# Optimization experiments

Hardware: AMD Instinct MI355X
Metric: run time of the kernel (lower is better)

## Reference

```python
import jax, jax.numpy as jnp
import numpy as np

B, T, D, V = 32, 512, 512, 512


def setup_inputs() -> dict:
    key = jax.random.key(0)
    k1, k2, k3, k4 = jax.random.split(key, 4)
    x = jax.random.normal(k1, (B, T, D), jnp.float32)
    proj_w = jax.random.normal(k2, (V, D), jnp.float32) * 0.02
    transitions = jax.random.normal(k3, (V, V), jnp.float32) * 0.02
    tgt_tokens = jax.random.randint(k4, (B, T), 0, V, dtype=jnp.int64)
    decoder_padding_mask = jnp.zeros((B, T), dtype=bool)  # all positions valid
    return {"x": x, "proj_w": proj_w, "transitions": transitions,
            "tgt_tokens": tgt_tokens, "decoder_padding_mask": decoder_padding_mask}


def reference(x, proj_w, transitions, tgt_tokens, decoder_padding_mask):
    # output projection (no bias): emissions [B,T,V]
    emissions = jnp.einsum('btd,vd->btv', x, proj_w)
    mask = (~decoder_padding_mask).astype(emissions.dtype)  # [B,T] word_ins_mask

    alpha0 = emissions[:, 0]                                # [B,V]
    emit_rest = jnp.swapaxes(emissions[:, 1:], 0, 1)        # [T-1,B,V]
    mask_rest = jnp.swapaxes(mask[:, 1:], 0, 1)             # [T-1,B]

    # ---- CRF forward algorithm (log partition) ----
    def fwd_step(alpha, inp):
        emit_t, m_t = inp
        # scores[b,i,j] = alpha[b,i] + trans[i,j] + emit_t[b,j]
        scores = alpha[:, :, None] + transitions[None, :, :] + emit_t[:, None, :]
        new = jax.nn.logsumexp(scores, axis=1)
        return jnp.where(m_t[:, None] > 0, new, alpha), None

    alpha_T, _ = jax.lax.scan(fwd_step, alpha0, (emit_rest, mask_rest))
    logZ = jax.nn.logsumexp(alpha_T, axis=-1)               # [B]

    # ---- gold path score ----
    emit_scores = jnp.take_along_axis(emissions, tgt_tokens[..., None], axis=-1)[..., 0]
    score = jnp.sum(emit_scores * mask, axis=-1)
    trans_scores = transitions[tgt_tokens[:, :-1], tgt_tokens[:, 1:]]  # [B,T-1]
    score = score + jnp.sum(trans_scores * mask[:, 1:] * mask[:, :-1], axis=-1)
    loglik = score - logZ                                   # [B]

    # ---- Viterbi decode ----
    lab = jnp.arange(V)

    def vit_step(alpha, inp):
        emit_t, m_t = inp
        scores = alpha[:, :, None] + transitions[None, :, :]  # [B,V,V]
        best_prev = jnp.argmax(scores, axis=1)                # [B,V]
        new = jnp.max(scores, axis=1) + emit_t
        alpha_new = jnp.where(m_t[:, None] > 0, new, alpha)
        bp = jnp.where(m_t[:, None] > 0, best_prev, lab[None, :])
        return alpha_new, bp

    valpha, bps = jax.lax.scan(vit_step, alpha0, (emit_rest, mask_rest))  # bps [T-1,B,V]
    last = jnp.argmax(valpha, axis=-1)                      # [B] token at T-1

    def back_step(tok_next, bp_t):
        tok_prev = jnp.take_along_axis(bp_t, tok_next[:, None], axis=1)[:, 0]
        return tok_prev, tok_next

    first, later = jax.lax.scan(back_step, last, bps, reverse=True)
    tokens = jnp.concatenate([first[:, None], jnp.swapaxes(later, 0, 1)], axis=1)  # [B,T]

    return emissions, loglik, tokens
```

## Files before the change

kernel.cpp:

```cpp
#include <hip/hip_runtime.h>

#define Bn 32
#define Tn 512
#define Dn 512
#define Vn 512

typedef float f4 __attribute__((ext_vector_type(4)));
typedef int i8v __attribute__((ext_vector_type(8)));
typedef _Float16 h8f __attribute__((ext_vector_type(8)));

__device__ __forceinline__ float max8lds(const float* p) {
  float4 a = *(const float4*)p;
  float4 b = *(const float4*)(p + 4);
  return fmaxf(fmaxf(fmaxf(a.x, a.y), fmaxf(a.z, a.w)),
               fmaxf(fmaxf(b.x, b.y), fmaxf(b.z, b.w)));
}

__device__ __forceinline__ float dpp64max(float x) {
  int t;
  t = __builtin_amdgcn_update_dpp(__float_as_int(x), __float_as_int(x), 0x111, 0xF, 0xF, false);
  x = fmaxf(x, __int_as_float(t));
  t = __builtin_amdgcn_update_dpp(__float_as_int(x), __float_as_int(x), 0x112, 0xF, 0xF, false);
  x = fmaxf(x, __int_as_float(t));
  t = __builtin_amdgcn_update_dpp(__float_as_int(x), __float_as_int(x), 0x114, 0xF, 0xF, false);
  x = fmaxf(x, __int_as_float(t));
  t = __builtin_amdgcn_update_dpp(__float_as_int(x), __float_as_int(x), 0x118, 0xF, 0xF, false);
  x = fmaxf(x, __int_as_float(t));
  t = __builtin_amdgcn_update_dpp(__float_as_int(x), __float_as_int(x), 0x142, 0xF, 0xF, false);
  x = fmaxf(x, __int_as_float(t));
  t = __builtin_amdgcn_update_dpp(__float_as_int(x), __float_as_int(x), 0x143, 0xF, 0xF, false);
  x = fmaxf(x, __int_as_float(t));
  return __int_as_float(__builtin_amdgcn_readlane(__float_as_int(x), 63));
}

__device__ __forceinline__ void bar_lgkm() {
  asm volatile("s_waitcnt lgkmcnt(0)" ::: "memory");
  __builtin_amdgcn_s_barrier();
}

__device__ __forceinline__ unsigned int f32_to_e4m3(float x) {
  x = fminf(x, 448.0f);
  unsigned int bits = __float_as_uint(x);
  int e = (int)((bits >> 23) & 0xFF) - 127;
  if (e < -6) {
    return (unsigned int)__float2int_rn(x * 512.0f);
  }
  unsigned int man = bits & 0x7FFFFF;
  int te = e + 7;
  unsigned int r = man >> 20;
  unsigned int rem = man & 0xFFFFF;
  if (rem > 0x80000u || (rem == 0x80000u && (r & 1u))) r++;
  if (r == 8u) { r = 0u; te++; }
  if (te > 15) { te = 15; r = 6u; }
  unsigned int byte = ((unsigned int)te << 3) | r;
  if (byte > 0x7Eu) byte = 0x7Eu;
  return byte;
}

__global__ __launch_bounds__(512) void crf_minmax(const float* __restrict__ trans,
                                                  unsigned int* __restrict__ Rout) {
  __shared__ float smn[8][64], smx[8][64];
  const int c = threadIdx.x & 63;
  const int seg = threadIdx.x >> 6;
  const int col = (int)blockIdx.x * 64 + c;
  float mn = 3e38f, mx = -3e38f;
#pragma unroll 4
  for (int u = seg * 64; u < seg * 64 + 64; ++u) {
    float t = trans[(size_t)u * Vn + col];
    mn = fminf(mn, t); mx = fmaxf(mx, t);
  }
  smn[seg][c] = mn; smx[seg][c] = mx;
  __syncthreads();
  if (seg == 0) {
#pragma unroll
    for (int i = 1; i < 8; ++i) { mn = fminf(mn, smn[i][c]); mx = fmaxf(mx, smx[i][c]); }
    float r = dpp64max(mx - mn);
    if (c == 0) atomicMax((int*)Rout, __float_as_int(r));
  }
}

__global__ __launch_bounds__(256) void crf_build_E8(const float* __restrict__ trans,
                                                    unsigned char* __restrict__ E8) {
  const int fid = (int)blockIdx.x;
  const int vt = fid >> 2, kc = fid & 3;
  const int t = threadIdx.x;
  const int lane = t >> 2;
  const int j0 = (t & 3) * 8;
  const int v = vt * 16 + (lane & 15);
  const int ubase = kc * 128 + (lane >> 4) * 32 + j0;
  unsigned long long pack = 0;
#pragma unroll
  for (int s = 0; s < 8; ++s) {
    float e = __expf(trans[(size_t)(ubase + s) * Vn + v]);
    pack |= (unsigned long long)f32_to_e4m3(e) << (8 * s);
  }
  *(unsigned long long*)(E8 + (size_t)fid * 2048 + lane * 32 + j0) = pack;
}

__global__ __launch_bounds__(256) void crf_gemm(const float* __restrict__ X,
                                                const float* __restrict__ Wt,
                                                float* __restrict__ C) {
  __shared__ h8f XfH[4][64], XfL[4][64];
  __shared__ h8f WfH[32][64], WfL[32][64];
  const int tid = threadIdx.x;
  const int m0 = (int)blockIdx.x * 64;
  const int wv = tid >> 6, lane = tid & 63;
  const int g = lane >> 4, cc = lane & 15;
  const int srow = tid >> 2;
  const int sc0 = (tid & 3) * 8;
  const int p = (tid & 3) * 16 + ((tid >> 2) & 15);
  f4 acc[32];
#pragma unroll
  for (int i = 0; i < 32; ++i) acc[i] = (f4)(0.f);

  for (int k0 = 0; k0 < Dn; k0 += 32) {
    __syncthreads();
    {
      const float* xp = X + (size_t)(m0 + srow) * Dn + k0 + sc0;
      float4 xa = *(const float4*)xp;
      float4 xb = *(const float4*)(xp + 4);
      float xs[8] = {xa.x, xa.y, xa.z, xa.w, xb.x, xb.y, xb.z, xb.w};
      _Float16 hh[8], ll[8];
#pragma unroll
      for (int i = 0; i < 8; ++i) {
        hh[i] = (_Float16)xs[i];
        ll[i] = (_Float16)(xs[i] - (float)hh[i]);
      }
      XfH[tid >> 6][p] = *(h8f*)hh;
      XfL[tid >> 6][p] = *(h8f*)ll;
#pragma unroll
      for (int i = 0; i < 8; ++i) {
        int r = i * 64 + srow;
        const float* wp = Wt + (size_t)r * Dn + k0 + sc0;
        float4 wa = *(const float4*)wp;
        float4 wb = *(const float4*)(wp + 4);
        float wsv[8] = {wa.x, wa.y, wa.z, wa.w, wb.x, wb.y, wb.z, wb.w};
        _Float16 wh[8], wl[8];
#pragma unroll
        for (int q = 0; q < 8; ++q) {
          wh[q] = (_Float16)wsv[q];
          wl[q] = (_Float16)(wsv[q] - (float)wh[q]);
        }
        WfH[i * 4 + (tid >> 6)][p] = *(h8f*)wh;
        WfL[i * 4 + (tid >> 6)][p] = *(h8f*)wl;
      }
    }
    __syncthreads();
    h8f aH = XfH[wv][lane];
    h8f aL = XfL[wv][lane];
#pragma unroll
    for (int nt = 0; nt < 32; ++nt) {
      h8f bH = WfH[nt][lane];
      h8f bL = WfL[nt][lane];
      acc[nt] = __builtin_amdgcn_mfma_f32_16x16x32_f16(aH, bH, acc[nt], 0, 0, 0);
      acc[nt] = __builtin_amdgcn_mfma_f32_16x16x32_f16(aH, bL, acc[nt], 0, 0, 0);
      acc[nt] = __builtin_amdgcn_mfma_f32_16x16x32_f16(aL, bH, acc[nt], 0, 0, 0);
      acc[nt] = __builtin_amdgcn_mfma_f32_16x16x32_f16(aL, bL, acc[nt], 0, 0, 0);
    }
  }
#pragma unroll
  for (int nt = 0; nt < 32; ++nt)
#pragma unroll
    for (int r = 0; r < 4; ++r)
      C[(size_t)(m0 + wv * 16 + 4 * g + r) * Vn + nt * 16 + cc] = acc[nt][r];
}

union SM {
  struct {
    __align__(16) unsigned char ph[Vn];
    __align__(16) float wred[8];
    __align__(16) float wred2[8];
    unsigned char padsh[Tn];
  } f;
  struct {
    __align__(16) float va2[2][Vn];
    __align__(16) unsigned short bpbuf[32][Vn];
    unsigned short tokens[Tn];
    __align__(16) float wvals[8];
    int widxs[8];
    unsigned char padsh[Tn];
    int lastS;
  } v;
};

__global__ __launch_bounds__(512, 2) void crf_scan(
    const float* __restrict__ emis, const float* __restrict__ trans,
    const unsigned char* __restrict__ E8, const float* __restrict__ Rp,
    const int* __restrict__ tgt, const unsigned char* __restrict__ pad,
    unsigned short* __restrict__ bps, float* __restrict__ out_ll,
    float* __restrict__ out_tok) {
  __shared__ SM sm;

  const int tid = threadIdx.x;
  const int b = blockIdx.x & 31;
  const int role = blockIdx.x >> 5;
  const float* eb = emis + (size_t)b * Tn * Vn;
  const int w = tid >> 6;
  const int lane = tid & 63;

  if (role == 0) {
    const int g = lane >> 4, c = lane & 15;
    const int t2sel = c >> 2, r2sel = c & 3;
    const int sidx = ((16 * ((lane >> 2) & 3)) + 4 * (lane >> 4) + (lane & 3)) << 2;
    i8v EA[4][4];
    {
      const i8v* E8v = (const i8v*)E8;
#pragma unroll
      for (int vt2 = 0; vt2 < 4; ++vt2)
#pragma unroll
        for (int kc = 0; kc < 4; ++kc)
          EA[vt2][kc] = E8v[((4 * w + vt2) * 4 + kc) * 64 + lane];
    }
    sm.f.padsh[tid] = pad[b * Tn + tid];
    float alphaR = eb[tid];
    float ecur = eb[Vn + tid];
    {
      float r = dpp64max(alphaR);
      if (lane == 0) sm.f.wred[w] = r;
    }
    bar_lgkm();
    float m = max8lds(sm.f.wred);

    for (int t = 1; t < Tn; ++t) {
      float p = __expf(alphaR - m);
      sm.f.ph[tid] = (unsigned char)f32_to_e4m3(p);
      bar_lgkm();
      float enext = (t + 1 < Tn) ? eb[(size_t)(t + 1) * Vn + tid] : 0.f;
      const uint4* phq = (const uint4*)sm.f.ph;
      i8v B4[4];
#pragma unroll
      for (int kc = 0; kc < 4; ++kc) {
        union { uint4 u[2]; i8v v; } bu;
        bu.u[0] = phq[kc * 8 + g * 2];
        bu.u[1] = phq[kc * 8 + g * 2 + 1];
        B4[kc] = bu.v;
      }
      f4 acc0 = (f4)(0.f), acc1 = (f4)(0.f), acc2 = (f4)(0.f), acc3 = (f4)(0.f);
#pragma unroll
      for (int kc = 0; kc < 4; ++kc) {
        acc0 = __builtin_amdgcn_mfma_scale_f32_16x16x128_f8f6f4(
            EA[0][kc], B4[kc], acc0, 0, 0, 0, 0x7F7F7F7F, 0, 0x7F7F7F7F);
        acc1 = __builtin_amdgcn_mfma_scale_f32_16x16x128_f8f6f4(
            EA[1][kc], B4[kc], acc1, 0, 0, 0, 0x7F7F7F7F, 0, 0x7F7F7F7F);
        acc2 = __builtin_amdgcn_mfma_scale_f32_16x16x128_f8f6f4(
            EA[2][kc], B4[kc], acc2, 0, 0, 0, 0x7F7F7F7F, 0, 0x7F7F7F7F);
        acc3 = __builtin_amdgcn_mfma_scale_f32_16x16x128_f8f6f4(
            EA[3][kc], B4[kc], acc3, 0, 0, 0, 0x7F7F7F7F, 0, 0x7F7F7F7F);
      }
      f4 at = (t2sel == 0) ? acc0 : (t2sel == 1) ? acc1 : (t2sel == 2) ? acc2 : acc3;
      float lo = (r2sel & 1) ? at[1] : at[0];
      float hi = (r2sel & 1) ? at[3] : at[2];
      float tot = (r2sel & 2) ? hi : lo;
      float tv = __int_as_float(__builtin_amdgcn_ds_bpermute(sidx, __float_as_int(tot)));
      float nv = m + __logf(tv) + ecur;
      if (sm.f.padsh[t]) nv = alphaR;
      alphaR = nv; ecur = enext;
      float rmx = dpp64max(nv);
      if (lane == 0) sm.f.wred[w] = rmx;
      bar_lgkm();
      m = max8lds(sm.f.wred);
    }

    __syncthreads();
    float ex = __expf(alphaR - m);
#pragma unroll
    for (int off = 1; off < 64; off <<= 1) ex += __shfl_xor(ex, off);
    if (lane == 0) sm.f.wred[w] = ex;
    float sc;
    {
      int t = tid;
      int tg = tgt[b * Tn + t];
      float mt = sm.f.padsh[t] ? 0.f : 1.f;
      sc = eb[(size_t)t * Vn + tg] * mt;
      if (t < Tn - 1) {
        int tg1 = tgt[b * Tn + t + 1];
        float mt1 = sm.f.padsh[t + 1] ? 0.f : 1.f;
        sc += trans[(size_t)tg * Vn + tg1] * mt * mt1;
      }
    }
#pragma unroll
    for (int off = 1; off < 64; off <<= 1) sc += __shfl_xor(sc, off);
    if (lane == 0) sm.f.wred2[w] = sc;
    __syncthreads();
    if (tid == 0) {
      float s = 0.f, gg = 0.f;
      for (int i = 0; i < 8; ++i) { s += sm.f.wred[i]; gg += sm.f.wred2[i]; }
      out_ll[b] = gg - (m + __logf(s));
    }
  } else {
    float R = __int_as_float(((const int*)Rp)[0]) * 1.000001f + 1e-4f;
    sm.v.padsh[tid] = pad[b * Tn + tid];
    float vaR = eb[tid];
    sm.v.va2[0][tid] = vaR;
    float ecur = eb[Vn + tid];
    bar_lgkm();

    for (int t = 1; t < Tn; ++t) {
      const int cur = t & 1, prev = cur ^ 1;
      const float* va2p = sm.v.va2[prev];
      const float4* vap4 = (const float4*)va2p;
      float4 q0 = vap4[lane * 2];
      float4 q1 = vap4[lane * 2 + 1];
      float mx8 = fmaxf(fmaxf(fmaxf(q0.x, q0.y), fmaxf(q0.z, q0.w)),
                        fmaxf(fmaxf(q1.x, q1.y), fmaxf(q1.z, q1.w)));
      float gmax = dpp64max(mx8);
      float thr = gmax - R;
      unsigned long long bm[8];
      bm[0] = __ballot(q0.x >= thr);
      bm[1] = __ballot(q0.y >= thr);
      bm[2] = __ballot(q0.z >= thr);
      bm[3] = __ballot(q0.w >= thr);
      bm[4] = __ballot(q1.x >= thr);
      bm[5] = __ballot(q1.y >= thr);
      bm[6] = __ballot(q1.z >= thr);
      bm[7] = __ballot(q1.w >= thr);
      unsigned long long any = bm[0] | bm[1] | bm[2] | bm[3] |
                               bm[4] | bm[5] | bm[6] | bm[7];
      float enext = (t + 1 < Tn) ? eb[(size_t)(t + 1) * Vn + tid] : 0.f;
      float best = -3e38f; int arg = 0;
      while (any) {
        int l = __ffsll(any) - 1; any &= any - 1;
#pragma unroll
        for (int j = 0; j < 8; ++j) {
          if ((bm[j] >> l) & 1) {
            int u = 8 * l + j;
            float cnd = va2p[u] + trans[(size_t)u * Vn + tid];
            if (cnd > best) { best = cnd; arg = u; }
          }
        }
      }
      float nv = best + ecur; int bp = arg;
      if (sm.v.padsh[t]) { nv = vaR; bp = tid; }
      bps[((size_t)(t - 1) * Bn + b) * Vn + tid] = (unsigned short)bp;
      sm.v.va2[cur][tid] = nv;
      vaR = nv; ecur = enext;
      bar_lgkm();
    }

    asm volatile("s_waitcnt vmcnt(0)" ::: "memory");
    __syncthreads();

    {
      float val = vaR;
      int idx = tid;
#pragma unroll
      for (int off = 1; off < 64; off <<= 1) {
        float ov = __shfl_xor(val, off);
        int oi = __shfl_xor(idx, off);
        if (ov > val || (ov == val && oi < idx)) { val = ov; idx = oi; }
      }
      if (lane == 0) { sm.v.wvals[w] = val; sm.v.widxs[w] = idx; }
    }
    __syncthreads();
    if (tid == 0) {
      float bv = sm.v.wvals[0]; int bi = sm.v.widxs[0];
      for (int i = 1; i < 8; ++i)
        if (sm.v.wvals[i] > bv || (sm.v.wvals[i] == bv && sm.v.widxs[i] < bi)) {
          bv = sm.v.wvals[i]; bi = sm.v.widxs[i];
        }
      sm.v.lastS = bi;
    }
    __syncthreads();
    int tok = sm.v.lastS;

    for (int cch = 15; cch >= 0; --cch) {
      int rhi = cch * 32 + 31; if (rhi > 510) rhi = 510;
      int srow = tid >> 4, part = tid & 15;
      int row = cch * 32 + srow;
      if (row <= 510) {
        const uint4* src = (const uint4*)(bps + ((size_t)row * Bn + b) * Vn);
        uint4* dst = (uint4*)&sm.v.bpbuf[srow][0];
#pragma unroll
        for (int qq = 0; qq < 4; ++qq) dst[part * 4 + qq] = src[part * 4 + qq];
      }
      __syncthreads();
      if (tid == 0) {
        int tk = tok;
        for (int rr = rhi; rr >= cch * 32; --rr) {
          sm.v.tokens[rr + 1] = (unsigned short)tk;
          tk = sm.v.bpbuf[rr - cch * 32][tk];
        }
        tok = tk;
      }
      __syncthreads();
    }
    if (tid == 0) sm.v.tokens[0] = (unsigned short)tok;
    __syncthreads();
    out_tok[b * Tn + tid] = (float)sm.v.tokens[tid];
  }
}

extern "C" void kernel_launch(void* const* d_in, const int* in_sizes, int n_in,
                              void* d_out, int out_size, void* d_ws, size_t ws_size,
                              hipStream_t stream) {
  const float* x = (const float*)d_in[0];
  const float* w = (const float*)d_in[1];
  const float* trans = (const float*)d_in[2];
  const int* tgt = (const int*)d_in[3];
  const unsigned char* pad = (const unsigned char*)d_in[4];
  float* out = (float*)d_out;

  char* ws = (char*)d_ws;
  float* Rp = (float*)ws;
  unsigned char* E8 = (unsigned char*)(ws + 64);
  unsigned short* bps = (unsigned short*)(ws + 64 + 524288);

  float* emis = out;
  float* out_ll = out + 8388608;
  float* out_tok = out + 8388640;

  (void)hipMemsetAsync(Rp, 0, 4, stream);
  hipLaunchKernelGGL(crf_minmax, dim3(8), dim3(512), 0, stream, trans, (unsigned int*)Rp);
  hipLaunchKernelGGL(crf_build_E8, dim3(128), dim3(256), 0, stream, trans, E8);
  hipLaunchKernelGGL(crf_gemm, dim3(256), dim3(256), 0, stream, x, w, emis);
  hipLaunchKernelGGL(crf_scan, dim3(64), dim3(512), 0, stream, emis, trans, E8, Rp,
                     tgt, pad, bps, out_ll, out_tok);
}
```

Measured before the change: 682.1 us.

## Run Viterbi scan in a single wavefront and use hardware fp8 convert

The Viterbi role now runs on one 64-lane wavefront. Each lane owns 8 states in registers, and LDS holds the alpha vector in a padded layout. This removes the per-step block barriers and lets each lane issue vectorized float4 transition loads and packed 16-byte backpointer stores. Backtracking is also done within the single wave without __syncthreads. Separately, the forward scan swaps the software e4m3 conversion for the hardware cvt_pk_fp8 builtin when it is available. The trade-off is that each Viterbi lane now does 8x the candidate work, and the other 7 waves of that block exit early.

```diff
diff --git a/kernel.cpp b/kernel.cpp
--- a/kernel.cpp
+++ b/kernel.cpp
@@ -55,6 +55,14 @@
   unsigned int byte = ((unsigned int)te << 3) | r;
   if (byte > 0x7Eu) byte = 0x7Eu;
   return byte;
+}
+
+__device__ __forceinline__ unsigned int cvt_e4m3_fast(float p) {
+#if __has_builtin(__builtin_amdgcn_cvt_pk_fp8_f32)
+  return (unsigned int)(__builtin_amdgcn_cvt_pk_fp8_f32(p, p, 0, false) & 0xFF);
+#else
+  return f32_to_e4m3(p);
+#endif
 }
 
 __global__ __launch_bounds__(512) void crf_minmax(const float* __restrict__ trans,
@@ -173,14 +181,11 @@
     unsigned char padsh[Tn];
   } f;
   struct {
-    __align__(16) float va2[2][Vn];
-    __align__(16) unsigned short bpbuf[32][Vn];
+    __align__(16) float va_lds[64 * 9];
+    __align__(16) unsigned short bpbuf[16][Vn];
     unsigned short tokens[Tn];
-    __align__(16) float wvals[8];
-    int widxs[8];
-    unsigned char padsh[Tn];
-    int lastS;
-  } v;
+    unsigned char padv[Tn];
+  } v1;
 };
 
 __global__ __launch_bounds__(512, 2) void crf_scan(
@@ -196,12 +201,12 @@
   const int role = blockIdx.x >> 5;
   const float* eb = emis + (size_t)b * Tn * Vn;
   const int w = tid >> 6;
-  const int lane = tid & 63;
+  const int lane64 = tid & 63;
 
   if (role == 0) {
-    const int g = lane >> 4, c = lane & 15;
+    const int g = lane64 >> 4, c = lane64 & 15;
     const int t2sel = c >> 2, r2sel = c & 3;
-    const int sidx = ((16 * ((lane >> 2) & 3)) + 4 * (lane >> 4) + (lane & 3)) << 2;
+    const int sidx = ((16 * ((lane64 >> 2) & 3)) + 4 * (lane64 >> 4) + (lane64 & 3)) << 2;
     i8v EA[4][4];
     {
       const i8v* E8v = (const i8v*)E8;
@@ -209,21 +214,21 @@
       for (int vt2 = 0; vt2 < 4; ++vt2)
 #pragma unroll
         for (int kc = 0; kc < 4; ++kc)
-          EA[vt2][kc] = E8v[((4 * w + vt2) * 4 + kc) * 64 + lane];
+          EA[vt2][kc] = E8v[((4 * w + vt2) * 4 + kc) * 64 + lane64];
     }
     sm.f.padsh[tid] = pad[b * Tn + tid];
     float alphaR = eb[tid];
     float ecur = eb[Vn + tid];
     {
       float r = dpp64max(alphaR);
-      if (lane == 0) sm.f.wred[w] = r;
+      if (lane64 == 0) sm.f.wred[w] = r;
     }
     bar_lgkm();
     float m = max8lds(sm.f.wred);
 
     for (int t = 1; t < Tn; ++t) {
       float p = __expf(alphaR - m);
-      sm.f.ph[tid] = (unsigned char)f32_to_e4m3(p);
+      sm.f.ph[tid] = (unsigned char)cvt_e4m3_fast(p);
       bar_lgkm();
       float enext = (t + 1 < Tn) ? eb[(size_t)(t + 1) * Vn + tid] : 0.f;
       const uint4* phq = (const uint4*)sm.f.ph;
@@ -256,7 +261,7 @@
       if (sm.f.padsh[t]) nv = alphaR;
       alphaR = nv; ecur = enext;
       float rmx = dpp64max(nv);
-      if (lane == 0) sm.f.wred[w] = rmx;
+      if (lane64 == 0) sm.f.wred[w] = rmx;
       bar_lgkm();
       m = max8lds(sm.f.wred);
     }
@@ -265,7 +270,7 @@
     float ex = __expf(alphaR - m);
 #pragma unroll
     for (int off = 1; off < 64; off <<= 1) ex += __shfl_xor(ex, off);
-    if (lane == 0) sm.f.wred[w] = ex;
+    if (lane64 == 0) sm.f.wred[w] = ex;
     float sc;
     {
       int t = tid;
@@ -280,7 +285,7 @@
     }
 #pragma unroll
     for (int off = 1; off < 64; off <<= 1) sc += __shfl_xor(sc, off);
-    if (lane == 0) sm.f.wred2[w] = sc;
+    if (lane64 == 0) sm.f.wred2[w] = sc;
     __syncthreads();
     if (tid == 0) {
       float s = 0.f, gg = 0.f;
@@ -288,105 +293,122 @@
       out_ll[b] = gg - (m + __logf(s));
     }
   } else {
+    if (tid >= 64) return;
+    const int lane = tid;
     float R = __int_as_float(((const int*)Rp)[0]) * 1.000001f + 1e-4f;
-    sm.v.padsh[tid] = pad[b * Tn + tid];
-    float vaR = eb[tid];
-    sm.v.va2[0][tid] = vaR;
-    float ecur = eb[Vn + tid];
-    bar_lgkm();
+#pragma unroll
+    for (int i = 0; i < 8; ++i)
+      sm.v1.padv[lane * 8 + i] = pad[b * Tn + lane * 8 + i];
+
+    float va[8], ecur[8], enext[8];
+    {
+      float4 a0 = *(const float4*)(eb + lane * 8);
+      float4 a1 = *(const float4*)(eb + lane * 8 + 4);
+      va[0] = a0.x; va[1] = a0.y; va[2] = a0.z; va[3] = a0.w;
+      va[4] = a1.x; va[5] = a1.y; va[6] = a1.z; va[7] = a1.w;
+      float4 e0 = *(const float4*)(eb + Vn + lane * 8);
+      float4 e1 = *(const float4*)(eb + Vn + lane * 8 + 4);
+      ecur[0] = e0.x; ecur[1] = e0.y; ecur[2] = e0.z; ecur[3] = e0.w;
+      ecur[4] = e1.x; ecur[5] = e1.y; ecur[6] = e1.z; ecur[7] = e1.w;
+#pragma unroll
+      for (int j = 0; j < 8; ++j) enext[j] = 0.f;
+    }
+#pragma unroll
+    for (int j = 0; j < 8; ++j) sm.v1.va_lds[9 * lane + j] = va[j];
 
     for (int t = 1; t < Tn; ++t) {
-      const int cur = t & 1, prev = cur ^ 1;
-      const float* va2p = sm.v.va2[prev];
-      const float4* vap4 = (const float4*)va2p;
-      float4 q0 = vap4[lane * 2];
-      float4 q1 = vap4[lane * 2 + 1];
-      float mx8 = fmaxf(fmaxf(fmaxf(q0.x, q0.y), fmaxf(q0.z, q0.w)),
-                        fmaxf(fmaxf(q1.x, q1.y), fmaxf(q1.z, q1.w)));
-      float gmax = dpp64max(mx8);
+      float mx = fmaxf(fmaxf(fmaxf(va[0], va[1]), fmaxf(va[2], va[3])),
+                       fmaxf(fmaxf(va[4], va[5]), fmaxf(va[6], va[7])));
+      float gmax = dpp64max(mx);
       float thr = gmax - R;
       unsigned long long bm[8];
-      bm[0] = __ballot(q0.x >= thr);
-      bm[1] = __ballot(q0.y >= thr);
-      bm[2] = __ballot(q0.z >= thr);
-      bm[3] = __ballot(q0.w >= thr);
-      bm[4] = __ballot(q1.x >= thr);
-      bm[5] = __ballot(q1.y >= thr);
-      bm[6] = __ballot(q1.z >= thr);
-      bm[7] = __ballot(q1.w >= thr);
+#pragma unroll
+      for (int j = 0; j < 8; ++j) bm[j] = __ballot(va[j] >= thr);
       unsigned long long any = bm[0] | bm[1] | bm[2] | bm[3] |
                                bm[4] | bm[5] | bm[6] | bm[7];
-      float enext = (t + 1 < Tn) ? eb[(size_t)(t + 1) * Vn + tid] : 0.f;
-      float best = -3e38f; int arg = 0;
+      if (t + 1 < Tn) {
+        float4 e0 = *(const float4*)(eb + (size_t)(t + 1) * Vn + lane * 8);
+        float4 e1 = *(const float4*)(eb + (size_t)(t + 1) * Vn + lane * 8 + 4);
+        enext[0] = e0.x; enext[1] = e0.y; enext[2] = e0.z; enext[3] = e0.w;
+        enext[4] = e1.x; enext[5] = e1.y; enext[6] = e1.z; enext[7] = e1.w;
+      }
+      float best[8]; int arg[8];
+#pragma unroll
+      for (int j = 0; j < 8; ++j) { best[j] = -3e38f; arg[j] = 0; }
       while (any) {
         int l = __ffsll(any) - 1; any &= any - 1;
 #pragma unroll
         for (int j = 0; j < 8; ++j) {
           if ((bm[j] >> l) & 1) {
             int u = 8 * l + j;
-            float cnd = va2p[u] + trans[(size_t)u * Vn + tid];
-            if (cnd > best) { best = cnd; arg = u; }
+            float vau = sm.v1.va_lds[9 * l + j];
+            const float* tr = trans + (size_t)u * Vn + lane * 8;
+            float4 t0 = *(const float4*)tr;
+            float4 t1 = *(const float4*)(tr + 4);
+            float cc0 = vau + t0.x, cc1 = vau + t0.y, cc2 = vau + t0.z, cc3 = vau + t0.w;
+            float cc4 = vau + t1.x, cc5 = vau + t1.y, cc6 = vau + t1.z, cc7 = vau + t1.w;
+            if (cc0 > best[0]) { best[0] = cc0; arg[0] = u; }
+            if (cc1 > best[1]) { best[1] = cc1; arg[1] = u; }
+            if (cc2 > best[2]) { best[2] = cc2; arg[2] = u; }
+            if (cc3 > best[3]) { best[3] = cc3; arg[3] = u; }
+            if (cc4 > best[4]) { best[4] = cc4; arg[4] = u; }
+            if (cc5 > best[5]) { best[5] = cc5; arg[5] = u; }
+            if (cc6 > best[6]) { best[6] = cc6; arg[6] = u; }
+            if (cc7 > best[7]) { best[7] = cc7; arg[7] = u; }
           }
         }
       }
-      float nv = best + ecur; int bp = arg;
-      if (sm.v.padsh[t]) { nv = vaR; bp = tid; }
-      bps[((size_t)(t - 1) * Bn + b) * Vn + tid] = (unsigned short)bp;
-      sm.v.va2[cur][tid] = nv;
-      vaR = nv; ecur = enext;
-      bar_lgkm();
+      bool pd = sm.v1.padv[t] != 0;
+      __align__(16) unsigned short bp8[8];
+#pragma unroll
+      for (int j = 0; j < 8; ++j) {
+        float nv = best[j] + ecur[j];
+        int bp = arg[j];
+        if (pd) { nv = va[j]; bp = 8 * lane + j; }
+        va[j] = nv;
+        bp8[j] = (unsigned short)bp;
+        ecur[j] = enext[j];
+      }
+      *(uint4*)(bps + ((size_t)(t - 1) * Bn + b) * Vn + lane * 8) = *(const uint4*)bp8;
+#pragma unroll
+      for (int j = 0; j < 8; ++j) sm.v1.va_lds[9 * lane + j] = va[j];
     }
 
     asm volatile("s_waitcnt vmcnt(0)" ::: "memory");
-    __syncthreads();
-
-    {
-      float val = vaR;
-      int idx = tid;
-#pragma unroll
-      for (int off = 1; off < 64; off <<= 1) {
-        float ov = __shfl_xor(val, off);
-        int oi = __shfl_xor(idx, off);
-        if (ov > val || (ov == val && oi < idx)) { val = ov; idx = oi; }
-      }
-      if (lane == 0) { sm.v.wvals[w] = val; sm.v.widxs[w] = idx; }
-    }
-    __syncthreads();
-    if (tid == 0) {
-      float bv = sm.v.wvals[0]; int bi = sm.v.widxs[0];
-      for (int i = 1; i < 8; ++i)
-        if (sm.v.wvals[i] > bv || (sm.v.wvals[i] == bv && sm.v.widxs[i] < bi)) {
-          bv = sm.v.wvals[i]; bi = sm.v.widxs[i];
+    float bv = va[0]; int bi = 8 * lane;
+#pragma unroll
+    for (int j = 1; j < 8; ++j)
+      if (va[j] > bv) { bv = va[j]; bi = 8 * lane + j; }
+#pragma unroll
+    for (int off = 1; off < 64; off <<= 1) {
+      float ov = __shfl_xor(bv, off);
+      int oi = __shfl_xor(bi, off);
+      if (ov > bv || (ov == bv && oi < bi)) { bv = ov; bi = oi; }
+    }
+    int tok = bi;
+
+    for (int cch = 31; cch >= 0; --cch) {
+      int rlo = cch * 16;
+      int rhi = rlo + 15; if (rhi > 510) rhi = 510;
+#pragma unroll
+      for (int rr = 0; rr < 16; ++rr) {
+        int row = cch * 16 + rr;
+        if (row <= 510) {
+          uint4 vdat = *(const uint4*)(bps + ((size_t)row * Bn + b) * Vn + lane * 8);
+          *(uint4*)&sm.v1.bpbuf[rr][lane * 8] = vdat;
         }
-      sm.v.lastS = bi;
-    }
-    __syncthreads();
-    int tok = sm.v.lastS;
-
-    for (int cch = 15; cch >= 0; --cch) {
-      int rhi = cch * 32 + 31; if (rhi > 510) rhi = 510;
-      int srow = tid >> 4, part = tid & 15;
-      int row = cch * 32 + srow;
-      if (row <= 510) {
-        const uint4* src = (const uint4*)(bps + ((size_t)row * Bn + b) * Vn);
-        uint4* dst = (uint4*)&sm.v.bpbuf[srow][0];
-#pragma unroll
-        for (int qq = 0; qq < 4; ++qq) dst[part * 4 + qq] = src[part * 4 + qq];
-      }
-      __syncthreads();
-      if (tid == 0) {
-        int tk = tok;
-        for (int rr = rhi; rr >= cch * 32; --rr) {
-          sm.v.tokens[rr + 1] = (unsigned short)tk;
-          tk = sm.v.bpbuf[rr - cch * 32][tk];
-        }
-        tok = tk;
-      }
-      __syncthreads();
-    }
-    if (tid == 0) sm.v.tokens[0] = (unsigned short)tok;
-    __syncthreads();
-    out_tok[b * Tn + tid] = (float)sm.v.tokens[tid];
+      }
+      asm volatile("s_waitcnt vmcnt(0) lgkmcnt(0)" ::: "memory");
+      for (int rr = rhi; rr >= rlo; --rr) {
+        if (lane == 0) sm.v1.tokens[rr + 1] = (unsigned short)tok;
+        tok = sm.v1.bpbuf[rr - rlo][tok];
+      }
+    }
+    if (lane == 0) sm.v1.tokens[0] = (unsigned short)tok;
+    asm volatile("s_waitcnt lgkmcnt(0)" ::: "memory");
+#pragma unroll
+    for (int i = 0; i < 8; ++i)
+      out_tok[b * Tn + lane * 8 + i] = (float)sm.v1.tokens[lane * 8 + i];
   }
 }
 
```

New measurement: 772.5 us. 1.13x slower.
